# Kernel tuning notes

Measured on AMD Instinct MI355X. Metric: run time of the kernel, lower is better.

## Reference

```python
import jax, jax.numpy as jnp
import numpy as np

N = 20000       # nodes
E = 320000      # edges
D_IN = 128
H = 512
OUT = 7
EPS = 1e-5


def setup_inputs() -> dict:
    key = jax.random.key(0)
    ks = jax.random.split(key, 16)
    def lin(k, fan_in, fan_out):
        bound = 1.0 / np.sqrt(fan_in)
        kw, kb = jax.random.split(k)
        W = jax.random.uniform(kw, (fan_in, fan_out), jnp.float32, -bound, bound)
        b = jax.random.uniform(kb, (fan_out,), jnp.float32, -bound, bound)
        return W, b
    x = jax.random.normal(ks[0], (N, D_IN), jnp.float32)
    edge_index = jax.random.randint(ks[1], (2, E), 0, N, dtype=jnp.int64)
    W1, b1 = lin(ks[2], D_IN, H)
    W2, b2 = lin(ks[3], H, H)
    W3, b3 = lin(ks[4], H, H)
    W4, b4 = lin(ks[5], H, H)
    ln_gamma = jnp.ones((H,), jnp.float32)
    ln_beta = jnp.zeros((H,), jnp.float32)
    W_out, b_out = lin(ks[6], H, OUT)
    return {"x": x, "edge_index": edge_index,
            "W1": W1, "b1": b1, "W2": W2, "b2": b2,
            "W3": W3, "b3": b3, "W4": W4, "b4": b4,
            "ln_gamma": ln_gamma, "ln_beta": ln_beta,
            "W_out": W_out, "b_out": b_out}


def _gcn_layer(x, W, b, src, dst, dinv):
    # transform, then symmetric-normalized gather/scatter-add (PyG GCNConv)
    h = x @ W                                    # [N, H]
    norm = dinv[src] * dinv[dst]                 # [E+N]
    msg = h[src] * norm[:, None]                 # gather + scale
    agg = jax.ops.segment_sum(msg, dst, num_segments=N)
    return agg + b


def reference(x, edge_index, W1, b1, W2, b2, W3, b3, W4, b4,
              ln_gamma, ln_beta, W_out, b_out):
    loops = jnp.arange(N, dtype=edge_index.dtype)
    src = jnp.concatenate([edge_index[0], loops])  # A + I self loops
    dst = jnp.concatenate([edge_index[1], loops])
    deg = jax.ops.segment_sum(jnp.ones_like(src, dtype=x.dtype), dst,
                              num_segments=N)
    dinv = jnp.where(deg > 0, jax.lax.rsqrt(deg), 0.0)

    def ln(h):
        mu = h.mean(-1, keepdims=True)
        var = h.var(-1, keepdims=True)
        return (h - mu) * jax.lax.rsqrt(var + EPS) * ln_gamma + ln_beta

    for W, b in ((W1, b1), (W2, b2), (W3, b3), (W4, b4)):
        x = jax.nn.relu(ln(_gcn_layer(x, W, b, src, dst, dinv)))
    g = x.mean(axis=0)           # mean pool over nodes -> [H]
    # dropout is identity in eval mode
    return g @ W_out + b_out     # [OUT]
```

## Files before the change

### kernel.cpp

```cpp
#include <hip/hip_runtime.h>

#define HID 512
#define OUTD 7
#define EPSV 1e-5f
#define PB 256

typedef __attribute__((ext_vector_type(8))) short bf16x8;
typedef __attribute__((ext_vector_type(4))) float f32x4;
typedef __attribute__((ext_vector_type(2))) float f32x2;
typedef unsigned short ushort_t;
typedef unsigned int uint_t;
typedef unsigned char uchar_t;

__device__ __forceinline__ ushort_t f2bf(float f) {
    uint_t u = __float_as_uint(f);
    u = (u + 0x7fffu + ((u >> 16) & 1u)) >> 16;
    return (ushort_t)u;
}
__device__ __forceinline__ float bflo(uint_t u) { return __uint_as_float(u << 16); }
__device__ __forceinline__ float bfhi(uint_t u) { return __uint_as_float(u & 0xffff0000u); }

__device__ __forceinline__ void dec4(uint_t v, float* f) {
    f32x2 p0 = __builtin_amdgcn_cvt_pk_f32_fp8(v, false);
    f32x2 p1 = __builtin_amdgcn_cvt_pk_f32_fp8(v, true);
    f[0] = p0.x; f[1] = p0.y; f[2] = p1.x; f[3] = p1.y;
}
__device__ __forceinline__ uint_t enc4(float a, float b, float c, float d) {
    uint_t r = __builtin_amdgcn_cvt_pk_fp8_f32(a, b, 0, false);
    r = __builtin_amdgcn_cvt_pk_fp8_f32(c, d, r, true);
    return r;
}

__device__ __forceinline__ void gload_lds16(const ushort_t* g, ushort_t* l) {
    __builtin_amdgcn_global_load_lds(
        (const __attribute__((address_space(1))) uint_t*)g,
        (__attribute__((address_space(3))) uint_t*)l, 16, 0, 0);
}
__device__ __forceinline__ void gload_lds16_u8(const uchar_t* g, uchar_t* l) {
    __builtin_amdgcn_global_load_lds(
        (const __attribute__((address_space(1))) uint_t*)g,
        (__attribute__((address_space(3))) uint_t*)l, 16, 0, 0);
}


__global__ void zero_deg(int* __restrict__ deg, int N) {
    int i = blockIdx.x * blockDim.x + threadIdx.x;
    if (i < N) deg[i] = 0;
}

__global__ void setup2(const int* __restrict__ dst, int* __restrict__ deg, int E,
                       const float* __restrict__ W0, const float* __restrict__ W1,
                       const float* __restrict__ W2, const float* __restrict__ W3,
                       ushort_t* __restrict__ T0, ushort_t* __restrict__ T1,
                       ushort_t* __restrict__ T2, ushort_t* __restrict__ T3) {
    int i = blockIdx.x * blockDim.x + threadIdx.x;
    if (i < E) { atomicAdd(&deg[dst[i]], 1); return; }
    i -= E;
    const int S0 = 128 * HID, S1 = HID * HID;
    if (i < S0) { int k = i / HID, n = i % HID; T0[(size_t)n * 128 + k] = f2bf(W0[i]); return; }
    i -= S0;
    if (i < S1) { int k = i / HID, n = i % HID; T1[(size_t)n * HID + k] = f2bf(W1[i]); return; }
    i -= S1;
    if (i < S1) { int k = i / HID, n = i % HID; T2[(size_t)n * HID + k] = f2bf(W2[i]); return; }
    i -= S1;
    if (i < S1) { int k = i / HID, n = i % HID; T3[(size_t)n * HID + k] = f2bf(W3[i]); }
}


__global__ void scan1(const int* __restrict__ deg, int* __restrict__ off,
                      int* __restrict__ partial, float* __restrict__ dinv, int N) {
    __shared__ int s[256];
    const int t = threadIdx.x;
    const int i = blockIdx.x * 256 + t;
    int d = (i < N) ? deg[i] : 0;
    if (i < N) dinv[i] = rsqrtf((float)(d + 1));
    s[t] = d;
    __syncthreads();
#pragma unroll
    for (int ofs = 1; ofs < 256; ofs <<= 1) {
        int v = (t >= ofs) ? s[t - ofs] : 0;
        __syncthreads();
        s[t] += v;
        __syncthreads();
    }
    if (i < N) off[i] = s[t] - d;
    if (t == 255) partial[blockIdx.x] = s[255];
}

__global__ void scan23(int* __restrict__ off, const int* __restrict__ partial,
                       int* __restrict__ cursor, int N, int E, int nb) {
    __shared__ int s[256];
    __shared__ int ex[256];
    const int t = threadIdx.x;
    int d = (t < nb) ? partial[t] : 0;
    s[t] = d;
    __syncthreads();
#pragma unroll
    for (int ofs = 1; ofs < 256; ofs <<= 1) {
        int v = (t >= ofs) ? s[t - ofs] : 0;
        __syncthreads();
        s[t] += v;
        __syncthreads();
    }
    ex[t] = s[t] - d;
    __syncthreads();
    int i = blockIdx.x * 256 + t;
    if (i < N) {
        int v = off[i] + ex[i >> 8];
        off[i] = v;
        cursor[i] = v;
    } else if (i == N) {
        off[N] = E;
    }
}


__global__ void fill_cvt(const int* __restrict__ src, const int* __restrict__ dst,
                         int* __restrict__ cursor, int* __restrict__ srcs, int E,
                         const float* __restrict__ x, const float* __restrict__ dinv,
                         ushort_t* __restrict__ xb, int pairs) {
    int i = blockIdx.x * blockDim.x + threadIdx.x;
    if (i < E) { int p = atomicAdd(&cursor[dst[i]], 1); srcs[p] = src[i]; return; }
    i -= E;
    if (i < pairs) {
        float dr = dinv[i >> 6];
        float a = x[2 * i] * dr, b = x[2 * i + 1] * dr;
        uint_t d = __builtin_amdgcn_cvt_pk_fp8_f32(a, b, 0, false);
        xb[i] = (ushort_t)(d & 0xffffu);
    }
}


__global__ __launch_bounds__(256) void csr_agg_512(
        const uchar_t* __restrict__ xs, const int* __restrict__ off,
        const int* __restrict__ srcs, const float* __restrict__ dinv,
        uchar_t* __restrict__ ax, int N) {
    int gtid = blockIdx.x * 256 + threadIdx.x;
    int r = gtid >> 6, lane = gtid & 63;
    if (r >= N) return;
    const int half = lane >> 5, l32 = lane & 31;
    const uint4* xb = (const uint4*)xs;
    float a[16];
    if (half == 0) {
        uint4 v = xb[(size_t)r * 32 + l32];
        dec4(v.x, a); dec4(v.y, a + 4); dec4(v.z, a + 8); dec4(v.w, a + 12);
    } else {
#pragma unroll
        for (int q = 0; q < 16; q++) a[q] = 0.f;
    }
    int e = off[r];
    const int e1 = off[r + 1];
    for (; e + 8 <= e1; e += 8) {
        int si[4]; uint4 vi[4];
#pragma unroll
        for (int j = 0; j < 4; j++) si[j] = srcs[e + 2 * j + half];
#pragma unroll
        for (int j = 0; j < 4; j++) vi[j] = xb[(size_t)si[j] * 32 + l32];
#pragma unroll
        for (int j = 0; j < 4; j++) {
            float f[16];
            dec4(vi[j].x, f); dec4(vi[j].y, f + 4); dec4(vi[j].z, f + 8); dec4(vi[j].w, f + 12);
#pragma unroll
            for (int q = 0; q < 16; q++) a[q] += f[q];
        }
    }
    for (; e < e1; e += 2) {
        int idx = e + half;
        bool valid = idx < e1;
        int s = srcs[valid ? idx : e];
        uint4 v = xb[(size_t)s * 32 + l32];
        if (!valid) { v.x = 0; v.y = 0; v.z = 0; v.w = 0; }
        float f[16];
        dec4(v.x, f); dec4(v.y, f + 4); dec4(v.z, f + 8); dec4(v.w, f + 12);
#pragma unroll
        for (int q = 0; q < 16; q++) a[q] += f[q];
    }
#pragma unroll
    for (int q = 0; q < 16; q++) a[q] += __shfl_xor(a[q], 32);
    if (half == 0) {
        float dr = dinv[r];
        uint4 o;
        o.x = enc4(a[0] * dr,  a[1] * dr,  a[2] * dr,  a[3] * dr);
        o.y = enc4(a[4] * dr,  a[5] * dr,  a[6] * dr,  a[7] * dr);
        o.z = enc4(a[8] * dr,  a[9] * dr,  a[10] * dr, a[11] * dr);
        o.w = enc4(a[12] * dr, a[13] * dr, a[14] * dr, a[15] * dr);
        ((uint4*)ax)[(size_t)r * 32 + l32] = o;
    }
}

__global__ __launch_bounds__(256) void csr_agg_128(
        const uchar_t* __restrict__ xs, const int* __restrict__ off,
        const int* __restrict__ srcs, const float* __restrict__ dinv,
        uchar_t* __restrict__ ax, int N) {
    int gtid = blockIdx.x * 256 + threadIdx.x;
    int r = gtid >> 6, lane = gtid & 63;
    if (r >= N) return;
    const int sub = lane >> 3, l8 = lane & 7;
    const uint4* xb = (const uint4*)xs;
    float a[16];
    if (sub == 0) {
        uint4 v = xb[(size_t)r * 8 + l8];
        dec4(v.x, a); dec4(v.y, a + 4); dec4(v.z, a + 8); dec4(v.w, a + 12);
    } else {
#pragma unroll
        for (int q = 0; q < 16; q++) a[q] = 0.f;
    }
    const int e1 = off[r + 1];
    for (int e = off[r]; e < e1; e += 8) {
        int idx = e + sub;
        bool valid = idx < e1;
        int s = srcs[valid ? idx : e];
        uint4 v = xb[(size_t)s * 8 + l8];
        if (!valid) { v.x = 0; v.y = 0; v.z = 0; v.w = 0; }
        float f[16];
        dec4(v.x, f); dec4(v.y, f + 4); dec4(v.z, f + 8); dec4(v.w, f + 12);
#pragma unroll
        for (int q = 0; q < 16; q++) a[q] += f[q];
    }
#pragma unroll
    for (int q = 0; q < 16; q++) a[q] += __shfl_xor(a[q], 8);
#pragma unroll
    for (int q = 0; q < 16; q++) a[q] += __shfl_xor(a[q], 16);
#pragma unroll
    for (int q = 0; q < 16; q++) a[q] += __shfl_xor(a[q], 32);
    if (sub == 0) {
        float dr = dinv[r];
        uint4 o;
        o.x = enc4(a[0] * dr,  a[1] * dr,  a[2] * dr,  a[3] * dr);
        o.y = enc4(a[4] * dr,  a[5] * dr,  a[6] * dr,  a[7] * dr);
        o.z = enc4(a[8] * dr,  a[9] * dr,  a[10] * dr, a[11] * dr);
        o.w = enc4(a[12] * dr, a[13] * dr, a[14] * dr, a[15] * dr);
        ((uint4*)ax)[(size_t)r * 8 + l8] = o;
    }
}


__global__ __launch_bounds__(256) void gemm_mfma(
        const uchar_t* __restrict__ A, const ushort_t* __restrict__ Wt,
        const float* __restrict__ bias, ushort_t* __restrict__ C, int M, int K) {
    __shared__ __align__(16) uchar_t  As[4 * 128 * 16];
    __shared__ __align__(16) ushort_t Bs[8 * 128 * 8];
    const int t = threadIdx.x;
    const int wave = t >> 6, lane = t & 63;
    const int m0 = blockIdx.y * 128, n0 = blockIdx.x * 128;
    const int wm = (wave & 1) * 64, wn = (wave >> 1) * 64;
    const int quad = lane >> 4, l16 = lane & 15;

    f32x4 acc[4][4];
#pragma unroll
    for (int i = 0; i < 4; i++)
#pragma unroll
        for (int j = 0; j < 4; j++) acc[i][j] = (f32x4){0.f, 0.f, 0.f, 0.f};

    for (int k0 = 0; k0 < K; k0 += 64) {
#pragma unroll
        for (int h = 0; h < 2; h++) {
            int gm = m0 + 64 * h + lane;
            if (gm >= M) gm = M - 1;
            gload_lds16_u8(A + (size_t)gm * K + k0 + wave * 16,
                           &As[(wave * 128 + 64 * h) * 16]);
        }
#pragma unroll
        for (int h = 0; h < 4; h++) {
            int cb = wave * 2 + (h >> 1);
            int row = (h & 1) * 64 + lane;
            gload_lds16(Wt + (size_t)(n0 + row) * K + k0 + cb * 8,
                        &Bs[(cb * 128 + (h & 1) * 64) * 8]);
        }
        __syncthreads();
#pragma unroll
        for (int kk = 0; kk < 2; kk++) {
            bf16x8 af[4], bfr[4];
#pragma unroll
            for (int jn = 0; jn < 4; jn++)
                bfr[jn] = *(const bf16x8*)&Bs[((kk * 4 + quad) * 128 + wn + jn * 16 + l16) * 8];
#pragma unroll
            for (int i = 0; i < 4; i++) {
                uint2 v8 = *(const uint2*)&As[((kk * 2 + (quad >> 1)) * 128 + wm + i * 16 + l16) * 16
                                              + (quad & 1) * 8];
                f32x2 p0 = __builtin_amdgcn_cvt_pk_f32_fp8(v8.x, false);
                f32x2 p1 = __builtin_amdgcn_cvt_pk_f32_fp8(v8.x, true);
                f32x2 p2 = __builtin_amdgcn_cvt_pk_f32_fp8(v8.y, false);
                f32x2 p3 = __builtin_amdgcn_cvt_pk_f32_fp8(v8.y, true);
                union { uint_t u[4]; bf16x8 v; } pk;
                pk.u[0] = (__float_as_uint(p0.y) & 0xffff0000u) | (__float_as_uint(p0.x) >> 16);
                pk.u[1] = (__float_as_uint(p1.y) & 0xffff0000u) | (__float_as_uint(p1.x) >> 16);
                pk.u[2] = (__float_as_uint(p2.y) & 0xffff0000u) | (__float_as_uint(p2.x) >> 16);
                pk.u[3] = (__float_as_uint(p3.y) & 0xffff0000u) | (__float_as_uint(p3.x) >> 16);
                af[i] = pk.v;
            }
#pragma unroll
            for (int i = 0; i < 4; i++)
#pragma unroll
                for (int jn = 0; jn < 4; jn++)
                    acc[i][jn] = __builtin_amdgcn_mfma_f32_16x16x32_bf16(
                                     af[i], bfr[jn], acc[i][jn], 0, 0, 0);
        }
        __syncthreads();
    }
#pragma unroll
    for (int i = 0; i < 4; i++) {
#pragma unroll
        for (int jn = 0; jn < 4; jn++) {
            int gn = n0 + wn + jn * 16 + l16;
            float bv = bias[gn];
#pragma unroll
            for (int rg = 0; rg < 4; rg++) {
                int gm = m0 + wm + i * 16 + quad * 4 + rg;
                if (gm < M) C[(size_t)gm * HID + gn] = f2bf(acc[i][jn][rg] + bv);
            }
        }
    }
}


__global__ void ln_relu(const ushort_t* __restrict__ h, const float* __restrict__ gamma,
                        const float* __restrict__ beta, const float* __restrict__ dinv,
                        void* __restrict__ optr, int N) {
    int gtid = blockIdx.x * blockDim.x + threadIdx.x;
    int r = gtid >> 6, lane = gtid & 63;
    if (r >= N) return;
    uint4 v = ((const uint4*)(h + (size_t)r * HID))[lane];
    float f[8] = {bflo(v.x), bfhi(v.x), bflo(v.y), bfhi(v.y),
                  bflo(v.z), bfhi(v.z), bflo(v.w), bfhi(v.w)};
    float s = 0.f, q = 0.f;
#pragma unroll
    for (int j = 0; j < 8; j++) { s += f[j]; q += f[j] * f[j]; }
#pragma unroll
    for (int ofs = 32; ofs > 0; ofs >>= 1) {
        s += __shfl_xor(s, ofs);
        q += __shfl_xor(q, ofs);
    }
    float mu  = s * (1.0f / HID);
    float var = q * (1.0f / HID) - mu * mu;
    float rs  = rsqrtf(var + EPSV);
    float dr  = dinv[r];
    const float4* gp = (const float4*)gamma;
    const float4* bp = (const float4*)beta;
    float4 g0 = gp[2 * lane], g1 = gp[2 * lane + 1];
    float4 b0 = bp[2 * lane], b1 = bp[2 * lane + 1];
    float gg[8] = {g0.x, g0.y, g0.z, g0.w, g1.x, g1.y, g1.z, g1.w};
    float bb[8] = {b0.x, b0.y, b0.z, b0.w, b1.x, b1.y, b1.z, b1.w};
    float o[8];
#pragma unroll
    for (int j = 0; j < 8; j++)
        o[j] = fmaxf((f[j] - mu) * rs * gg[j] + bb[j], 0.f) * dr;
    uint2 ov;
    ov.x = enc4(o[0], o[1], o[2], o[3]);
    ov.y = enc4(o[4], o[5], o[6], o[7]);
    ((uint2*)optr)[(size_t)r * 64 + lane] = ov;
}


__global__ __launch_bounds__(256) void ln_pool(
        const ushort_t* __restrict__ h, const float* __restrict__ gamma,
        const float* __restrict__ beta, float* __restrict__ pbuf, int N) {
    __shared__ float sred[4][64][8];
    const int t = threadIdx.x;
    const int sub = t >> 6, lane = t & 63;
    const float4* gp = (const float4*)gamma;
    const float4* bp = (const float4*)beta;
    float4 g0 = gp[2 * lane], g1 = gp[2 * lane + 1];
    float4 b0 = bp[2 * lane], b1 = bp[2 * lane + 1];
    float gg[8] = {g0.x, g0.y, g0.z, g0.w, g1.x, g1.y, g1.z, g1.w};
    float bb[8] = {b0.x, b0.y, b0.z, b0.w, b1.x, b1.y, b1.z, b1.w};
    float colacc[8] = {0.f, 0.f, 0.f, 0.f, 0.f, 0.f, 0.f, 0.f};
    const int step = PB * 4;
    for (int r = blockIdx.x * 4 + sub; r < N; r += step) {
        uint4 v = ((const uint4*)(h + (size_t)r * HID))[lane];
        float f[8] = {bflo(v.x), bfhi(v.x), bflo(v.y), bfhi(v.y),
                      bflo(v.z), bfhi(v.z), bflo(v.w), bfhi(v.w)};
        float s = 0.f, q = 0.f;
#pragma unroll
        for (int j = 0; j < 8; j++) { s += f[j]; q += f[j] * f[j]; }
#pragma unroll
        for (int ofs = 32; ofs > 0; ofs >>= 1) {
            s += __shfl_xor(s, ofs);
            q += __shfl_xor(q, ofs);
        }
        float mu  = s * (1.0f / HID);
        float var = q * (1.0f / HID) - mu * mu;
        float rs  = rsqrtf(var + EPSV);
#pragma unroll
        for (int j = 0; j < 8; j++)
            colacc[j] += fmaxf((f[j] - mu) * rs * gg[j] + bb[j], 0.f);
    }
#pragma unroll
    for (int j = 0; j < 8; j++) sred[sub][lane][j] = colacc[j];
    __syncthreads();
    if (sub == 0) {
        float4 o0, o1;
        o0.x = sred[0][lane][0] + sred[1][lane][0] + sred[2][lane][0] + sred[3][lane][0];
        o0.y = sred[0][lane][1] + sred[1][lane][1] + sred[2][lane][1] + sred[3][lane][1];
        o0.z = sred[0][lane][2] + sred[1][lane][2] + sred[2][lane][2] + sred[3][lane][2];
        o0.w = sred[0][lane][3] + sred[1][lane][3] + sred[2][lane][3] + sred[3][lane][3];
        o1.x = sred[0][lane][4] + sred[1][lane][4] + sred[2][lane][4] + sred[3][lane][4];
        o1.y = sred[0][lane][5] + sred[1][lane][5] + sred[2][lane][5] + sred[3][lane][5];
        o1.z = sred[0][lane][6] + sred[1][lane][6] + sred[2][lane][6] + sred[3][lane][6];
        o1.w = sred[0][lane][7] + sred[1][lane][7] + sred[2][lane][7] + sred[3][lane][7];
        float* pb = pbuf + (size_t)blockIdx.x * HID + lane * 8;
        ((float4*)pb)[0] = o0;
        ((float4*)pb)[1] = o1;
    }
}


__global__ void out_kernel(const float* __restrict__ pbuf, const float* __restrict__ Wout,
                           const float* __restrict__ bout, float* __restrict__ out, int N) {
    __shared__ float red[256];
    int t = threadIdx.x;
    float g0 = 0.f, g1 = 0.f;
    for (int p = 0; p < PB; p += 4) {
#pragma unroll
        for (int u = 0; u < 4; u++) {
            const float2 v = ((const float2*)(pbuf + (size_t)(p + u) * HID))[t];
            g0 += v.x; g1 += v.y;
        }
    }
    float invn = 1.0f / (float)N;
    for (int o = 0; o < OUTD; o++) {
        float pr = g0 * Wout[(2 * t) * OUTD + o] + g1 * Wout[(2 * t + 1) * OUTD + o];
        red[t] = pr;
        __syncthreads();
        for (int sft = 128; sft > 0; sft >>= 1) {
            if (t < sft) red[t] += red[t + sft];
            __syncthreads();
        }
        if (t == 0) out[o] = red[0] * invn + bout[o];
        __syncthreads();
    }
}


extern "C" void kernel_launch(void* const* d_in, const int* in_sizes, int n_in,
                              void* d_out, int out_size, void* d_ws, size_t ws_size,
                              hipStream_t stream) {
    const float* x  = (const float*)d_in[0];
    const int*   ei = (const int*)d_in[1];
    const int N = in_sizes[0] / 128;
    const int E = in_sizes[1] / 2;
    const int* src = ei;
    const int* dst = ei + E;
    const float* Ws[4] = {(const float*)d_in[2], (const float*)d_in[4],
                          (const float*)d_in[6], (const float*)d_in[8]};
    const float* bs[4] = {(const float*)d_in[3], (const float*)d_in[5],
                          (const float*)d_in[7], (const float*)d_in[9]};
    const float* gamma = (const float*)d_in[10];
    const float* beta  = (const float*)d_in[11];
    const float* Wout  = (const float*)d_in[12];
    const float* bout  = (const float*)d_in[13];
    float* out = (float*)d_out;

    char* p = (char*)d_ws;
    uchar_t*  axb = (uchar_t*)p;   p += (size_t)N * HID;
    ushort_t* hb  = (ushort_t*)p;  p += sizeof(ushort_t) * (size_t)N * HID;
    uchar_t*  ho8 = (uchar_t*)p;   p += (size_t)N * HID;
    uchar_t*  xb8 = ho8;
    ushort_t* Wt[4];
    Wt[0] = (ushort_t*)p;          p += sizeof(ushort_t) * 128 * HID;
    Wt[1] = (ushort_t*)p;          p += sizeof(ushort_t) * HID * HID;
    Wt[2] = (ushort_t*)p;          p += sizeof(ushort_t) * HID * HID;
    Wt[3] = (ushort_t*)p;          p += sizeof(ushort_t) * HID * HID;
    float* dinv = (float*)p;       p += sizeof(float) * N;
    float* pbuf = (float*)p;       p += sizeof(float) * PB * HID;
    int* deg    = (int*)p;         p += sizeof(int) * N;
    int* off    = (int*)p;         p += sizeof(int) * (N + 4);
    int* cursor = (int*)p;         p += sizeof(int) * N;
    int* partial= (int*)p;         p += sizeof(int) * 256;
    int* srcs   = (int*)p;

    const int nb = (N + 255) / 256;

    zero_deg<<<(N + 255) / 256, 256, 0, stream>>>(deg, N);
    {
        int tot = E + 128 * HID + 3 * HID * HID;
        setup2<<<(tot + 255) / 256, 256, 0, stream>>>(dst, deg, E, Ws[0], Ws[1], Ws[2], Ws[3],
                                                      Wt[0], Wt[1], Wt[2], Wt[3]);
    }
    scan1<<<nb, 256, 0, stream>>>(deg, off, partial, dinv, N);
    scan23<<<(N + 256) / 256, 256, 0, stream>>>(off, partial, cursor, N, E, nb);
    {
        int pairs = N * 64;
        int tot = E + pairs;
        fill_cvt<<<(tot + 255) / 256, 256, 0, stream>>>(src, dst, cursor, srcs, E,
                                                        x, dinv, (ushort_t*)xb8, pairs);
    }

    for (int l = 0; l < 4; l++) {
        const int K = (l == 0) ? 128 : HID;
        if (l == 0)
            csr_agg_128<<<(N * 64 + 255) / 256, 256, 0, stream>>>(xb8, off, srcs, dinv, axb, N);
        else
            csr_agg_512<<<(N * 64 + 255) / 256, 256, 0, stream>>>(ho8, off, srcs, dinv, axb, N);
        dim3 gg(HID / 128, (N + 127) / 128);
        gemm_mfma<<<gg, 256, 0, stream>>>(axb, Wt[l], bs[l], hb, N, K);
        if (l < 3)
            ln_relu<<<(N * 64 + 255) / 256, 256, 0, stream>>>(hb, gamma, beta, dinv, ho8, N);
        else
            ln_pool<<<PB, 256, 0, stream>>>(hb, gamma, beta, pbuf, N);
    }
    out_kernel<<<1, 256, 0, stream>>>(pbuf, Wout, bout, out, N);
}
```

Baseline: 391.2 us.

## Fuse GEMM with LayerNorm+ReLU epilogue using full-row 64x512 tiles

Replaces the 128x128-tile GEMM plus separate ln_relu/ln_pool kernels with one kernel in which each 512-thread block computes a full 64-row by 512-column output tile. Row mean and variance are reduced in-block, and the epilogue either writes fp8 LayerNorm+ReLU+dinv-scaled output through an LDS transpose or produces per-block column sums for pooling. This removes the bf16 intermediate round trip to global memory and two kernel launches per layer. In exchange, each block must load the whole weight matrix for every k-step, using more LDS (64KB B tile), and the grid has fewer, larger blocks, which may lower occupancy.

```diff
diff --git a/kernel.cpp b/kernel.cpp
--- a/kernel.cpp
+++ b/kernel.cpp
@@ -3,7 +3,6 @@
 #define HID 512
 #define OUTD 7
 #define EPSV 1e-5f
-#define PB 256
 
 typedef __attribute__((ext_vector_type(8))) short bf16x8;
 typedef __attribute__((ext_vector_type(4))) float f32x4;
@@ -29,6 +28,9 @@
     uint_t r = __builtin_amdgcn_cvt_pk_fp8_f32(a, b, 0, false);
     r = __builtin_amdgcn_cvt_pk_fp8_f32(c, d, r, true);
     return r;
+}
+__device__ __forceinline__ uchar_t enc1(float a) {
+    return (uchar_t)(__builtin_amdgcn_cvt_pk_fp8_f32(a, a, 0, false) & 0xffu);
 }
 
 __device__ __forceinline__ void gload_lds16(const ushort_t* g, ushort_t* l) {
@@ -235,17 +237,31 @@
 }
 
 
-__global__ __launch_bounds__(256) void gemm_mfma(
+template<int MODE>
+__global__ __launch_bounds__(512) void gemm_ln(
         const uchar_t* __restrict__ A, const ushort_t* __restrict__ Wt,
-        const float* __restrict__ bias, ushort_t* __restrict__ C, int M, int K) {
-    __shared__ __align__(16) uchar_t  As[4 * 128 * 16];
-    __shared__ __align__(16) ushort_t Bs[8 * 128 * 8];
+        const float* __restrict__ bias, const float* __restrict__ gamma,
+        const float* __restrict__ beta, const float* __restrict__ dinv,
+        void* __restrict__ outp, int M, int K) {
+    __shared__ __align__(16) uchar_t  As[4 * 64 * 16];
+    __shared__ __align__(16) ushort_t Bs[8 * 512 * 8];
+    __shared__ float ssum[64][8], ssq[64][8];
+    __shared__ float muv[64], rsv[64], drow[64];
     const int t = threadIdx.x;
     const int wave = t >> 6, lane = t & 63;
-    const int m0 = blockIdx.y * 128, n0 = blockIdx.x * 128;
-    const int wm = (wave & 1) * 64, wn = (wave >> 1) * 64;
+    const int m0 = blockIdx.x * 64;
+    const int wn = wave * 64;
     const int quad = lane >> 4, l16 = lane & 15;
 
+    if (MODE == 0 && t < 64) drow[t] = dinv[min(m0 + t, M - 1)];
+
+    float bb4[4], gv4[4], bv4[4];
+#pragma unroll
+    for (int jn = 0; jn < 4; jn++) {
+        int col = wn + jn * 16 + l16;
+        bb4[jn] = bias[col]; gv4[jn] = gamma[col]; bv4[jn] = beta[col];
+    }
+
     f32x4 acc[4][4];
 #pragma unroll
     for (int i = 0; i < 4; i++)
@@ -253,30 +269,27 @@
         for (int j = 0; j < 4; j++) acc[i][j] = (f32x4){0.f, 0.f, 0.f, 0.f};
 
     for (int k0 = 0; k0 < K; k0 += 64) {
-#pragma unroll
-        for (int h = 0; h < 2; h++) {
-            int gm = m0 + 64 * h + lane;
+        if (wave < 4) {
+            int gm = m0 + lane;
             if (gm >= M) gm = M - 1;
-            gload_lds16_u8(A + (size_t)gm * K + k0 + wave * 16,
-                           &As[(wave * 128 + 64 * h) * 16]);
-        }
-#pragma unroll
-        for (int h = 0; h < 4; h++) {
-            int cb = wave * 2 + (h >> 1);
-            int row = (h & 1) * 64 + lane;
-            gload_lds16(Wt + (size_t)(n0 + row) * K + k0 + cb * 8,
-                        &Bs[(cb * 128 + (h & 1) * 64) * 8]);
-        }
-        __syncthreads();
-#pragma unroll
-        for (int kk = 0; kk < 2; kk++) {
+            gload_lds16_u8(A + (size_t)gm * K + k0 + wave * 16, &As[(wave * 64) * 16]);
+        }
+#pragma unroll
+        for (int h = 0; h < 8; h++) {
+            int row = h * 64 + lane;
+            gload_lds16(Wt + (size_t)row * K + k0 + wave * 8,
+                        &Bs[(wave * 512 + h * 64) * 8]);
+        }
+        __syncthreads();
+#pragma unroll
+        for (int ks = 0; ks < 2; ks++) {
             bf16x8 af[4], bfr[4];
 #pragma unroll
             for (int jn = 0; jn < 4; jn++)
-                bfr[jn] = *(const bf16x8*)&Bs[((kk * 4 + quad) * 128 + wn + jn * 16 + l16) * 8];
+                bfr[jn] = *(const bf16x8*)&Bs[((ks * 4 + quad) * 512 + wn + jn * 16 + l16) * 8];
 #pragma unroll
             for (int i = 0; i < 4; i++) {
-                uint2 v8 = *(const uint2*)&As[((kk * 2 + (quad >> 1)) * 128 + wm + i * 16 + l16) * 16
+                uint2 v8 = *(const uint2*)&As[((ks * 2 + (quad >> 1)) * 64 + i * 16 + l16) * 16
                                               + (quad & 1) * 8];
                 f32x2 p0 = __builtin_amdgcn_cvt_pk_f32_fp8(v8.x, false);
                 f32x2 p1 = __builtin_amdgcn_cvt_pk_f32_fp8(v8.x, true);
@@ -298,124 +311,110 @@
         }
         __syncthreads();
     }
+
+#pragma unroll
+    for (int i = 0; i < 4; i++)
+#pragma unroll
+        for (int jn = 0; jn < 4; jn++)
+#pragma unroll
+            for (int rg = 0; rg < 4; rg++)
+                acc[i][jn][rg] += bb4[jn];
+
 #pragma unroll
     for (int i = 0; i < 4; i++) {
 #pragma unroll
+        for (int rg = 0; rg < 4; rg++) {
+            float s = acc[i][0][rg] + acc[i][1][rg] + acc[i][2][rg] + acc[i][3][rg];
+            float q = acc[i][0][rg] * acc[i][0][rg] + acc[i][1][rg] * acc[i][1][rg]
+                    + acc[i][2][rg] * acc[i][2][rg] + acc[i][3][rg] * acc[i][3][rg];
+            s += __shfl_xor(s, 1); q += __shfl_xor(q, 1);
+            s += __shfl_xor(s, 2); q += __shfl_xor(q, 2);
+            s += __shfl_xor(s, 4); q += __shfl_xor(q, 4);
+            s += __shfl_xor(s, 8); q += __shfl_xor(q, 8);
+            if (l16 == 0) {
+                int row = i * 16 + quad * 4 + rg;
+                ssum[row][wave] = s;
+                ssq[row][wave] = q;
+            }
+        }
+    }
+    __syncthreads();
+    if (t < 64) {
+        float s = 0.f, q = 0.f;
+#pragma unroll
+        for (int w = 0; w < 8; w++) { s += ssum[t][w]; q += ssq[t][w]; }
+        float mu = s * (1.0f / HID);
+        float var = q * (1.0f / HID) - mu * mu;
+        muv[t] = mu;
+        rsv[t] = rsqrtf(var + EPSV);
+    }
+    __syncthreads();
+
+    if (MODE == 0) {
+        uchar_t* trbuf = (uchar_t*)Bs;
+#pragma unroll
+        for (int i = 0; i < 4; i++) {
+#pragma unroll
+            for (int rg = 0; rg < 4; rg++) {
+                int row = i * 16 + quad * 4 + rg;
+                float mu = muv[row], rs = rsv[row], dr = drow[row];
+#pragma unroll
+                for (int jn = 0; jn < 4; jn++) {
+                    float val = fmaxf((acc[i][jn][rg] - mu) * rs * gv4[jn] + bv4[jn], 0.f) * dr;
+                    trbuf[row * 516 + wn + jn * 16 + l16] = enc1(val);
+                }
+            }
+        }
+        __syncthreads();
+        const uint_t* tr32 = (const uint_t*)Bs;
+        uint_t* gout = (uint_t*)outp;
+#pragma unroll
+        for (int it = 0; it < 16; it++) {
+            int gidx = it * 512 + t;
+            int row = gidx >> 7, dwi = gidx & 127;
+            if (m0 + row < M)
+                gout[(size_t)(m0 + row) * 128 + dwi] = tr32[row * 129 + dwi];
+        }
+    } else {
+        float colacc[4] = {0.f, 0.f, 0.f, 0.f};
+#pragma unroll
+        for (int i = 0; i < 4; i++) {
+#pragma unroll
+            for (int rg = 0; rg < 4; rg++) {
+                int row = i * 16 + quad * 4 + rg;
+                bool valid = (m0 + row) < M;
+                float mu = muv[row], rs = rsv[row];
+#pragma unroll
+                for (int jn = 0; jn < 4; jn++) {
+                    float val = fmaxf((acc[i][jn][rg] - mu) * rs * gv4[jn] + bv4[jn], 0.f);
+                    colacc[jn] += valid ? val : 0.f;
+                }
+            }
+        }
+#pragma unroll
         for (int jn = 0; jn < 4; jn++) {
-            int gn = n0 + wn + jn * 16 + l16;
-            float bv = bias[gn];
-#pragma unroll
-            for (int rg = 0; rg < 4; rg++) {
-                int gm = m0 + wm + i * 16 + quad * 4 + rg;
-                if (gm < M) C[(size_t)gm * HID + gn] = f2bf(acc[i][jn][rg] + bv);
-            }
-        }
-    }
-}
-
-
-__global__ void ln_relu(const ushort_t* __restrict__ h, const float* __restrict__ gamma,
-                        const float* __restrict__ beta, const float* __restrict__ dinv,
-                        void* __restrict__ optr, int N) {
-    int gtid = blockIdx.x * blockDim.x + threadIdx.x;
-    int r = gtid >> 6, lane = gtid & 63;
-    if (r >= N) return;
-    uint4 v = ((const uint4*)(h + (size_t)r * HID))[lane];
-    float f[8] = {bflo(v.x), bfhi(v.x), bflo(v.y), bfhi(v.y),
-                  bflo(v.z), bfhi(v.z), bflo(v.w), bfhi(v.w)};
-    float s = 0.f, q = 0.f;
-#pragma unroll
-    for (int j = 0; j < 8; j++) { s += f[j]; q += f[j] * f[j]; }
-#pragma unroll
-    for (int ofs = 32; ofs > 0; ofs >>= 1) {
-        s += __shfl_xor(s, ofs);
-        q += __shfl_xor(q, ofs);
-    }
-    float mu  = s * (1.0f / HID);
-    float var = q * (1.0f / HID) - mu * mu;
-    float rs  = rsqrtf(var + EPSV);
-    float dr  = dinv[r];
-    const float4* gp = (const float4*)gamma;
-    const float4* bp = (const float4*)beta;
-    float4 g0 = gp[2 * lane], g1 = gp[2 * lane + 1];
-    float4 b0 = bp[2 * lane], b1 = bp[2 * lane + 1];
-    float gg[8] = {g0.x, g0.y, g0.z, g0.w, g1.x, g1.y, g1.z, g1.w};
-    float bb[8] = {b0.x, b0.y, b0.z, b0.w, b1.x, b1.y, b1.z, b1.w};
-    float o[8];
-#pragma unroll
-    for (int j = 0; j < 8; j++)
-        o[j] = fmaxf((f[j] - mu) * rs * gg[j] + bb[j], 0.f) * dr;
-    uint2 ov;
-    ov.x = enc4(o[0], o[1], o[2], o[3]);
-    ov.y = enc4(o[4], o[5], o[6], o[7]);
-    ((uint2*)optr)[(size_t)r * 64 + lane] = ov;
-}
-
-
-__global__ __launch_bounds__(256) void ln_pool(
-        const ushort_t* __restrict__ h, const float* __restrict__ gamma,
-        const float* __restrict__ beta, float* __restrict__ pbuf, int N) {
-    __shared__ float sred[4][64][8];
-    const int t = threadIdx.x;
-    const int sub = t >> 6, lane = t & 63;
-    const float4* gp = (const float4*)gamma;
-    const float4* bp = (const float4*)beta;
-    float4 g0 = gp[2 * lane], g1 = gp[2 * lane + 1];
-    float4 b0 = bp[2 * lane], b1 = bp[2 * lane + 1];
-    float gg[8] = {g0.x, g0.y, g0.z, g0.w, g1.x, g1.y, g1.z, g1.w};
-    float bb[8] = {b0.x, b0.y, b0.z, b0.w, b1.x, b1.y, b1.z, b1.w};
-    float colacc[8] = {0.f, 0.f, 0.f, 0.f, 0.f, 0.f, 0.f, 0.f};
-    const int step = PB * 4;
-    for (int r = blockIdx.x * 4 + sub; r < N; r += step) {
-        uint4 v = ((const uint4*)(h + (size_t)r * HID))[lane];
-        float f[8] = {bflo(v.x), bfhi(v.x), bflo(v.y), bfhi(v.y),
-                      bflo(v.z), bfhi(v.z), bflo(v.w), bfhi(v.w)};
-        float s = 0.f, q = 0.f;
-#pragma unroll
-        for (int j = 0; j < 8; j++) { s += f[j]; q += f[j] * f[j]; }
-#pragma unroll
-        for (int ofs = 32; ofs > 0; ofs >>= 1) {
-            s += __shfl_xor(s, ofs);
-            q += __shfl_xor(q, ofs);
-        }
-        float mu  = s * (1.0f / HID);
-        float var = q * (1.0f / HID) - mu * mu;
-        float rs  = rsqrtf(var + EPSV);
-#pragma unroll
-        for (int j = 0; j < 8; j++)
-            colacc[j] += fmaxf((f[j] - mu) * rs * gg[j] + bb[j], 0.f);
-    }
-#pragma unroll
-    for (int j = 0; j < 8; j++) sred[sub][lane][j] = colacc[j];
-    __syncthreads();
-    if (sub == 0) {
-        float4 o0, o1;
-        o0.x = sred[0][lane][0] + sred[1][lane][0] + sred[2][lane][0] + sred[3][lane][0];
-        o0.y = sred[0][lane][1] + sred[1][lane][1] + sred[2][lane][1] + sred[3][lane][1];
-        o0.z = sred[0][lane][2] + sred[1][lane][2] + sred[2][lane][2] + sred[3][lane][2];
-        o0.w = sred[0][lane][3] + sred[1][lane][3] + sred[2][lane][3] + sred[3][lane][3];
-        o1.x = sred[0][lane][4] + sred[1][lane][4] + sred[2][lane][4] + sred[3][lane][4];
-        o1.y = sred[0][lane][5] + sred[1][lane][5] + sred[2][lane][5] + sred[3][lane][5];
-        o1.z = sred[0][lane][6] + sred[1][lane][6] + sred[2][lane][6] + sred[3][lane][6];
-        o1.w = sred[0][lane][7] + sred[1][lane][7] + sred[2][lane][7] + sred[3][lane][7];
-        float* pb = pbuf + (size_t)blockIdx.x * HID + lane * 8;
-        ((float4*)pb)[0] = o0;
-        ((float4*)pb)[1] = o1;
+            colacc[jn] += __shfl_xor(colacc[jn], 16);
+            colacc[jn] += __shfl_xor(colacc[jn], 32);
+        }
+        if (quad == 0) {
+            float* pb = (float*)outp + (size_t)blockIdx.x * HID;
+#pragma unroll
+            for (int jn = 0; jn < 4; jn++)
+                pb[wn + jn * 16 + l16] = colacc[jn];
+        }
     }
 }
 
 
 __global__ void out_kernel(const float* __restrict__ pbuf, const float* __restrict__ Wout,
-                           const float* __restrict__ bout, float* __restrict__ out, int N) {
+                           const float* __restrict__ bout, float* __restrict__ out,
+                           int N, int MB) {
     __shared__ float red[256];
     int t = threadIdx.x;
     float g0 = 0.f, g1 = 0.f;
-    for (int p = 0; p < PB; p += 4) {
-#pragma unroll
-        for (int u = 0; u < 4; u++) {
-            const float2 v = ((const float2*)(pbuf + (size_t)(p + u) * HID))[t];
-            g0 += v.x; g1 += v.y;
-        }
+    for (int p = 0; p < MB; p++) {
+        const float2 v = ((const float2*)(pbuf + (size_t)p * HID))[t];
+        g0 += v.x; g1 += v.y;
     }
     float invn = 1.0f / (float)N;
     for (int o = 0; o < OUTD; o++) {
@@ -451,9 +450,10 @@
     const float* bout  = (const float*)d_in[13];
     float* out = (float*)d_out;
 
+    const int MB = (N + 63) / 64;
+
     char* p = (char*)d_ws;
     uchar_t*  axb = (uchar_t*)p;   p += (size_t)N * HID;
-    ushort_t* hb  = (ushort_t*)p;  p += sizeof(ushort_t) * (size_t)N * HID;
     uchar_t*  ho8 = (uchar_t*)p;   p += (size_t)N * HID;
     uchar_t*  xb8 = ho8;
     ushort_t* Wt[4];
@@ -462,7 +462,7 @@
     Wt[2] = (ushort_t*)p;          p += sizeof(ushort_t) * HID * HID;
     Wt[3] = (ushort_t*)p;          p += sizeof(ushort_t) * HID * HID;
     float* dinv = (float*)p;       p += sizeof(float) * N;
-    float* pbuf = (float*)p;       p += sizeof(float) * PB * HID;
+    float* pbuf = (float*)p;       p += sizeof(float) * (size_t)MB * HID;
     int* deg    = (int*)p;         p += sizeof(int) * N;
     int* off    = (int*)p;         p += sizeof(int) * (N + 4);
     int* cursor = (int*)p;         p += sizeof(int) * N;
@@ -492,12 +492,12 @@
             csr_agg_128<<<(N * 64 + 255) / 256, 256, 0, stream>>>(xb8, off, srcs, dinv, axb, N);
         else
             csr_agg_512<<<(N * 64 + 255) / 256, 256, 0, stream>>>(ho8, off, srcs, dinv, axb, N);
-        dim3 gg(HID / 128, (N + 127) / 128);
-        gemm_mfma<<<gg, 256, 0, stream>>>(axb, Wt[l], bs[l], hb, N, K);
         if (l < 3)
-            ln_relu<<<(N * 64 + 255) / 256, 256, 0, stream>>>(hb, gamma, beta, dinv, ho8, N);
+            gemm_ln<0><<<MB, 512, 0, stream>>>(axb, Wt[l], bs[l], gamma, beta, dinv,
+                                               ho8, N, K);
         else
-            ln_pool<<<PB, 256, 0, stream>>>(hb, gamma, beta, pbuf, N);
-    }
-    out_kernel<<<1, 256, 0, stream>>>(pbuf, Wout, bout, out, N);
-}
+            gemm_ln<1><<<MB, 512, 0, stream>>>(axb, Wt[l], bs[l], gamma, beta, dinv,
+                                               pbuf, N, K);
+    }
+    out_kernel<<<1, 256, 0, stream>>>(pbuf, Wout, bout, out, N, MB);
+}
```

Measured after the change: 484.8 us. +23.9%, slower.
